# Kernel optimization log

Hardware: AMD Instinct MI355X
Metric: run time of the kernel (lower is better)

Reference implementation:

```python
import jax, jax.numpy as jnp
import numpy as np

NF = 64            # n_filter
CFAC = 3           # SinSobel c_factor: identity + sobel-x + sobel-y
FIN = NF * CFAC    # dyna block input channels (192)
FH = NF * 2        # dyna hidden (128)
FOUT = NF          # dyna output (64)
LAT = 512
N_CALLS = 6        # ceil(log2(128) - log2(2))
P_SIZES = [FH * FIN, FH, FH * FH, FH, FOUT * FH, FOUT, FOUT * FIN, FOUT]
P_TOTAL = sum(P_SIZES)  # 61824
_OFFS = np.cumsum([0] + P_SIZES)

def act(t):
    return jax.nn.leaky_relu(t, 0.2)

def conv1x1(x, w, b):
    # x [B,I,H,W], w [O,I] -> [B,O,H,W]
    return jnp.einsum('bihw,oi->bohw', x, w) + b[None, :, None, None]

def res_block(x, w0, b0, w1, b1):
    # GAN-stability style residual block with 1x1 convs
    return x + 0.1 * conv1x1(act(conv1x1(act(x), w0, b0)), w1, b1)

def depthwise3x3(x, k2d):
    C = x.shape[1]
    k = jnp.broadcast_to(k2d.astype(x.dtype), (C, 1, 3, 3))
    return jax.lax.conv_general_dilated(
        x, k, (1, 1), [(1, 1), (1, 1)],
        dimension_numbers=('NCHW', 'OIHW', 'NCHW'),
        feature_group_count=C)

SOBEL_X = jnp.array([[1., 0., -1.], [2., 0., -2.], [1., 0., -1.]], jnp.float32) / 8.0
SOBEL_Y = SOBEL_X.T
_g = jnp.exp(-0.5 * jnp.array([-1., 0., 1.], jnp.float32) ** 2)
GAUSS = jnp.outer(_g, _g)
GAUSS = GAUSS / GAUSS.sum()

def sin_sobel(x):
    return jnp.concatenate([x, depthwise3x3(x, SOBEL_X), depthwise3x3(x, SOBEL_Y)], axis=1)

def dyna_residual(x, params):
    # per-sample hypernetwork-generated 1x1-conv residual block
    B = x.shape[0]
    def take(i, shape):
        return params[:, _OFFS[i]:_OFFS[i + 1]].reshape((B,) + shape)
    w_in, b_in = take(0, (FH, FIN)), take(1, (FH,))
    w_mid, b_mid = take(2, (FH, FH)), take(3, (FH,))
    w_out, b_out = take(4, (FOUT, FH)), take(5, (FOUT,))
    w_sk, b_sk = take(6, (FOUT, FIN)), take(7, (FOUT,))
    def pconv(h, w, b):  # batched per-sample 1x1 conv
        return jnp.einsum('bihw,boi->bohw', h, w) + b[:, :, None, None]
    x_s = pconv(x, w_sk, b_sk)
    dx = pconv(x, w_in, b_in)
    dx = pconv(act(dx), w_mid, b_mid)
    dx = pconv(act(dx), w_out, b_out)
    return x_s + dx

def downsample(x):
    # GaussianSmoothing(k=3, sigma=1, pad=1) then bilinear 0.5
    # (align_corners=False bilinear at scale 0.5 == 2x2 average pooling)
    x = depthwise3x3(x, GAUSS)
    B, C, H, W = x.shape
    return x.reshape(B, C, H // 2, 2, W // 2, 2).mean(axis=(3, 5))

def lin_res(x, w1, b1, w2, b2, sw=None, sb=None):
    x_s = x if sw is None else x @ sw + sb
    return x_s + 0.1 * (act(act(x) @ w1 + b1) @ w2 + b2)

def forward(x, inj_lat, leak, in_w, in_b, inrb_w0, inrb_b0, inrb_w1, inrb_b1,
            hyp_w, hyp_b, outrb_w0, outrb_b0, outrb_w1, outrb_b1,
            l1_sw, l1_sb, l1_w1, l1_b1, l1_w2, l1_b2,
            l2_w1, l2_b1, l2_w2, l2_b2, lo_w, lo_b):
    out = conv1x1(x, in_w, in_b)
    out = res_block(out, inrb_w0, inrb_b0, inrb_w1, inrb_b1)
    leak_f = jnp.clip(leak, 0.001, 1000.0)
    dyn_params = inj_lat @ hyp_w + hyp_b  # [B, P_TOTAL], shared across calls
    out_embs = [out]
    for _ in range(N_CALLS):  # fixed small layer loop; spatial dims halve each call
        out_new = sin_sobel(out)
        out_new = dyna_residual(out_new, dyn_params)
        out = out + leak_f * out_new
        out = downsample(out)
        out_embs.append(out)
    out = res_block(out, outrb_w0, outrb_b0, outrb_w1, outrb_b1)
    h = out.mean(axis=(2, 3))  # [B, NF]
    h = lin_res(h, l1_w1, l1_b1, l1_w2, l1_b2, l1_sw, l1_sb)
    h = lin_res(h, l2_w1, l2_b1, l2_w2, l2_b2)
    lat = h @ lo_w + lo_b
    return lat, out_embs

def setup_inputs() -> dict:
    key = jax.random.key(0)
    ks = jax.random.split(key, 24)
    B, C, S = 8, 3, 128
    def rn(k, shape, scale=0.05):
        return scale * jax.random.normal(k, shape, jnp.float32)
    z = lambda n: jnp.zeros((n,), jnp.float32)
    return {
        'x': jax.random.normal(ks[0], (B, C, S, S), jnp.float32),
        'inj_lat': jax.random.normal(ks[1], (B, LAT), jnp.float32),
        'leak': jnp.array(0.1, jnp.float32),
        'in_w': rn(ks[2], (NF, C)), 'in_b': z(NF),
        'inrb_w0': rn(ks[3], (NF, NF)), 'inrb_b0': z(NF),
        'inrb_w1': rn(ks[4], (NF, NF)), 'inrb_b1': z(NF),
        'hyp_w': rn(ks[5], (LAT, P_TOTAL), 0.01), 'hyp_b': rn(ks[6], (P_TOTAL,), 0.01),
        'outrb_w0': rn(ks[7], (NF, NF)), 'outrb_b0': z(NF),
        'outrb_w1': rn(ks[8], (NF, NF)), 'outrb_b1': z(NF),
        'l1_sw': rn(ks[9], (NF, LAT)), 'l1_sb': z(LAT),
        'l1_w1': rn(ks[10], (NF, 2 * LAT)), 'l1_b1': z(2 * LAT),
        'l1_w2': rn(ks[11], (2 * LAT, LAT)), 'l1_b2': z(LAT),
        'l2_w1': rn(ks[12], (LAT, LAT)), 'l2_b1': z(LAT),
        'l2_w2': rn(ks[13], (LAT, LAT)), 'l2_b2': z(LAT),
        'lo_w': rn(ks[14], (LAT, LAT)), 'lo_b': z(LAT),
    }

def reference(x, inj_lat, leak, in_w, in_b, inrb_w0, inrb_b0, inrb_w1, inrb_b1,
              hyp_w, hyp_b, outrb_w0, outrb_b0, outrb_w1, outrb_b1,
              l1_sw, l1_sb, l1_w1, l1_b1, l1_w2, l1_b2,
              l2_w1, l2_b1, l2_w2, l2_b2, lo_w, lo_b):
    lat, out_embs = forward(x, inj_lat, leak, in_w, in_b, inrb_w0, inrb_b0, inrb_w1, inrb_b1,
                            hyp_w, hyp_b, outrb_w0, outrb_b0, outrb_w1, outrb_b1,
                            l1_sw, l1_sb, l1_w1, l1_b1, l1_w2, l1_b2,
                            l2_w1, l2_b1, l2_w2, l2_b2, lo_w, lo_b)
    return (lat, *out_embs)
```

## Files before the change

### kernel.cpp

```cpp
#include <hip/hip_runtime.h>


#define BATCH 8
#define PT 61824

typedef __attribute__((ext_vector_type(8))) short bf16x8;
typedef __attribute__((ext_vector_type(4))) float f32x4;

__device__ __forceinline__ float lrelu(float v) { return v > 0.f ? v : 0.2f * v; }

__device__ __forceinline__ short f2bf(float f) {
    union { float fv; unsigned u; } v; v.fv = f;
    return (short)((v.u + 0x7fffu + ((v.u >> 16) & 1u)) >> 16);
}

__global__ __launch_bounds__(256) void hyper_kernel(
    const float* __restrict__ inj, const float* __restrict__ hw,
    const float* __restrict__ hb, float* __restrict__ dyn,
    short* __restrict__ dyn16)
{
    __shared__ float s_l[512 * 8];
    int t = threadIdx.x;
    for (int i = t; i < 4096; i += 256) {
        int b = i >> 9, k = i & 511;
        s_l[k * 8 + b] = inj[i];
    }
    __syncthreads();
    int p = blockIdx.x * 256 + t;
    if (p >= PT) return;
    float acc[8];
#pragma unroll
    for (int b = 0; b < 8; ++b) acc[b] = 0.f;
    for (int k = 0; k < 512; ++k) {
        float w = hw[(size_t)k * PT + p];
        float4 a0 = *(const float4*)&s_l[k * 8];
        float4 a1 = *(const float4*)&s_l[k * 8 + 4];
        acc[0] += a0.x * w; acc[1] += a0.y * w; acc[2] += a0.z * w; acc[3] += a0.w * w;
        acc[4] += a1.x * w; acc[5] += a1.y * w; acc[6] += a1.z * w; acc[7] += a1.w * w;
    }
    float bias = hb[p];
#pragma unroll
    for (int b = 0; b < 8; ++b) {
        float v = acc[b] + bias;
        dyn[(size_t)b * PT + p] = v;
        dyn16[(size_t)b * PT + p] = f2bf(v);
    }
}

__global__ __launch_bounds__(256) void stem_kernel(
    const float* __restrict__ x, const float* __restrict__ in_w,
    const float* __restrict__ in_b,
    const float* __restrict__ w0, const float* __restrict__ b0,
    const float* __restrict__ w1, const float* __restrict__ b1,
    float* __restrict__ out0)
{
    const int HW = 128 * 128;
    __shared__ float s_t0[64 * 68];
    __shared__ short s_vh[2 * 64 * 72];
    __shared__ float s_x[192];
    short* s_v = s_vh;
    short* s_h = s_vh + 64 * 72;
    float* s_y = (float*)s_vh;

    const int b = blockIdx.x >> 8;
    const int tile = blockIdx.x & 255;
    const int pix0 = tile * 64;
    const int t = threadIdx.x;
    const int l = t & 63, w = t >> 6;
    const int lp = l & 15, lq = l >> 4;

    if (t < 192) s_x[t] = x[(size_t)b * 3 * HW + (t >> 6) * HW + pix0 + (t & 63)];
    __syncthreads();

    for (int j = t; j < 1024; j += 256) {
        int p = j & 63, cg = j >> 6;
        float x0 = s_x[p], x1 = s_x[64 + p], x2 = s_x[128 + p];
        short pk[4];
#pragma unroll
        for (int cc = 0; cc < 4; ++cc) {
            int c = cg * 4 + cc;
            float v = in_b[c] + x0 * in_w[c * 3] + x1 * in_w[c * 3 + 1]
                    + x2 * in_w[c * 3 + 2];
            s_t0[c * 68 + p] = v;
            pk[cc] = f2bf(lrelu(v));
        }
        *(short4*)&s_v[p * 72 + cg * 4] = make_short4(pk[0], pk[1], pk[2], pk[3]);
    }
    __syncthreads();

    const int o = w * 16 + lp;
    const f32x4 z4 = {0.f, 0.f, 0.f, 0.f};

    bf16x8 wb0[2], wb1[2];
#pragma unroll
    for (int k = 0; k < 2; ++k) {
        bf16x8 p0, p1;
#pragma unroll
        for (int e = 0; e < 8; ++e) {
            p0[e] = f2bf(w0[o * 64 + k * 32 + lq * 8 + e]);
            p1[e] = f2bf(w1[o * 64 + k * 32 + lq * 8 + e]);
        }
        wb0[k] = p0; wb1[k] = p1;
    }

    {
        f32x4 acc[4];
#pragma unroll
        for (int mt = 0; mt < 4; ++mt) acc[mt] = z4;
#pragma unroll
        for (int k = 0; k < 2; ++k)
#pragma unroll
            for (int mt = 0; mt < 4; ++mt) {
                bf16x8 a = *(const bf16x8*)&s_v[(mt * 16 + lp) * 72 + k * 32 + lq * 8];
                acc[mt] = __builtin_amdgcn_mfma_f32_16x16x32_bf16(a, wb0[k], acc[mt], 0, 0, 0);
            }
        float bi = b0[o];
#pragma unroll
        for (int mt = 0; mt < 4; ++mt)
#pragma unroll
            for (int r = 0; r < 4; ++r)
                s_h[(mt * 16 + lq * 4 + r) * 72 + o] = f2bf(lrelu(acc[mt][r] + bi));
    }
    __syncthreads();

    {
        f32x4 acc[4];
#pragma unroll
        for (int mt = 0; mt < 4; ++mt) acc[mt] = z4;
#pragma unroll
        for (int k = 0; k < 2; ++k)
#pragma unroll
            for (int mt = 0; mt < 4; ++mt) {
                bf16x8 a = *(const bf16x8*)&s_h[(mt * 16 + lp) * 72 + k * 32 + lq * 8];
                acc[mt] = __builtin_amdgcn_mfma_f32_16x16x32_bf16(a, wb1[k], acc[mt], 0, 0, 0);
            }
        float bi = b1[o];
        __syncthreads();
#pragma unroll
        for (int mt = 0; mt < 4; ++mt) {
            f32x4 dv;
#pragma unroll
            for (int r = 0; r < 4; ++r) dv[r] = 0.1f * (acc[mt][r] + bi);
            *(f32x4*)&s_y[o * 68 + mt * 16 + lq * 4] = dv;
        }
    }
    __syncthreads();

#pragma unroll
    for (int v = 0; v < 4; ++v) {
        int idx = v * 1024 + t * 4;
        int oo = idx >> 6, px = idx & 63;
        f32x4 t0v = *(const f32x4*)&s_t0[oo * 68 + px];
        f32x4 dv = *(const f32x4*)&s_y[oo * 68 + px];
        f32x4 ov = t0v + dv;
        *(f32x4*)&out0[((size_t)b * 64 + oo) * HW + pix0 + px] = ov;
    }
}

template<int MT>
__global__ __launch_bounds__(256) void iter_kernel(
    const float* __restrict__ cur, const float* __restrict__ dynf,
    const short* __restrict__ dynb, const float* __restrict__ leak_p,
    float* __restrict__ y, int S, int sh)
{
    constexpr int PX = MT * 16;
    constexpr int SY = (MT == 4) ? 68 : 20;
    __shared__ short s_s[PX * 200];
    __shared__ short s_h[PX * 136];
    float* s_y = (float*)s_s;

    const int HW = S * S;
    const int tilesPer = HW / PX;
    const int b = blockIdx.x / tilesPer;
    const int tile = blockIdx.x - b * tilesPer;
    const int pix0 = tile * PX;
    const int t = threadIdx.x;
    const int l = t & 63, w = t >> 6;
    const int lp = l & 15, lq = l >> 4;
    const float* base = cur + (size_t)b * 64 * HW;

    {
        const int p = (MT == 4) ? (lp + 16 * w) : lp;
        const int gpx = pix0 + p;
        const int row = gpx >> sh;
        const int x = gpx & (S - 1);
        const bool rm = (row > 0), rp = (row < S - 1);
        const bool le = (lp == 0) && (x > 0);
        const bool re = (lp == 15) && (x < S - 1);
        const int iters = (MT == 4) ? 8 : 2;
        int* s32 = (int*)s_s;
        for (int i = 0; i < iters; ++i) {
            const int cp = (MT == 4) ? (lq + 4 * i) : (lq + 4 * w + 16 * i);
            unsigned pk_id = 0, pk_sx = 0, pk_sy = 0;
#pragma unroll
            for (int cc = 0; cc < 2; ++cc) {
                const int c = 2 * cp + cc;
                const float* ch = base + (size_t)c * HW + row * S;
                float vm = rm ? ch[x - S] : 0.f;
                float v0 = ch[x];
                float vp = rp ? ch[x + S] : 0.f;
                float elm = 0.f, el0 = 0.f, elp = 0.f, erm = 0.f, er0 = 0.f, erp = 0.f;
                if (le) { elm = rm ? ch[x - 1 - S] : 0.f; el0 = ch[x - 1]; elp = rp ? ch[x - 1 + S] : 0.f; }
                if (re) { erm = rm ? ch[x + 1 - S] : 0.f; er0 = ch[x + 1]; erp = rp ? ch[x + 1 + S] : 0.f; }
                float Lm = __shfl(vm, l - 1), L0 = __shfl(v0, l - 1), Lp = __shfl(vp, l - 1);
                float Rm = __shfl(vm, l + 1), R0 = __shfl(v0, l + 1), Rp = __shfl(vp, l + 1);
                if (lp == 0)  { Lm = elm; L0 = el0; Lp = elp; }
                if (lp == 15) { Rm = erm; R0 = er0; Rp = erp; }
                if (x == 0)     { Lm = 0.f; L0 = 0.f; Lp = 0.f; }
                if (x == S - 1) { Rm = 0.f; R0 = 0.f; Rp = 0.f; }
                float sx = (Lm - Rm + 2.f * (L0 - R0) + Lp - Rp) * 0.125f;
                float sy = (Lm + 2.f * vm + Rm - Lp - 2.f * vp - Rp) * 0.125f;
                unsigned hid = (unsigned short)f2bf(v0);
                unsigned hsx = (unsigned short)f2bf(sx);
                unsigned hsy = (unsigned short)f2bf(sy);
                pk_id |= hid << (16 * cc);
                pk_sx |= hsx << (16 * cc);
                pk_sy |= hsy << (16 * cc);
            }
            s32[p * 100 + cp] = (int)pk_id;
            s32[p * 100 + 32 + cp] = (int)pk_sx;
            s32[p * 100 + 64 + cp] = (int)pk_sy;
        }
    }
    __syncthreads();

    const short* wb = dynb + (size_t)b * PT;
    const float* pf = dynf + (size_t)b * PT;
    const f32x4 z4 = {0.f, 0.f, 0.f, 0.f};

    f32x4 acc_sk[MT];
#pragma unroll
    for (int mt = 0; mt < MT; ++mt) acc_sk[mt] = z4;

    {
        f32x4 acc[2][MT];
#pragma unroll
        for (int n = 0; n < 2; ++n)
#pragma unroll
            for (int mt = 0; mt < MT; ++mt) acc[n][mt] = z4;
        const int osk = w * 16 + lp;
        for (int k = 0; k < 6; ++k) {
            bf16x8 a[MT];
#pragma unroll
            for (int mt = 0; mt < MT; ++mt)
                a[mt] = *(const bf16x8*)&s_s[(mt * 16 + lp) * 200 + k * 32 + lq * 8];
#pragma unroll
            for (int n = 0; n < 2; ++n) {
                int o = (w * 2 + n) * 16 + lp;
                bf16x8 bb = *(const bf16x8*)&wb[o * 192 + k * 32 + lq * 8];
#pragma unroll
                for (int mt = 0; mt < MT; ++mt)
                    acc[n][mt] = __builtin_amdgcn_mfma_f32_16x16x32_bf16(a[mt], bb, acc[n][mt], 0, 0, 0);
            }
            {
                bf16x8 bsk = *(const bf16x8*)&wb[49472 + osk * 192 + k * 32 + lq * 8];
#pragma unroll
                for (int mt = 0; mt < MT; ++mt)
                    acc_sk[mt] = __builtin_amdgcn_mfma_f32_16x16x32_bf16(a[mt], bsk, acc_sk[mt], 0, 0, 0);
            }
        }
#pragma unroll
        for (int n = 0; n < 2; ++n) {
            int o = (w * 2 + n) * 16 + lp;
            float bi = pf[24576 + o];
#pragma unroll
            for (int mt = 0; mt < MT; ++mt)
#pragma unroll
                for (int r = 0; r < 4; ++r)
                    s_h[(mt * 16 + lq * 4 + r) * 136 + o] = f2bf(lrelu(acc[n][mt][r] + bi));
        }
    }
    __syncthreads();

    {
        f32x4 acc[2][MT];
#pragma unroll
        for (int n = 0; n < 2; ++n)
#pragma unroll
            for (int mt = 0; mt < MT; ++mt) acc[n][mt] = z4;
        for (int k = 0; k < 4; ++k) {
            bf16x8 a[MT];
#pragma unroll
            for (int mt = 0; mt < MT; ++mt)
                a[mt] = *(const bf16x8*)&s_h[(mt * 16 + lp) * 136 + k * 32 + lq * 8];
#pragma unroll
            for (int n = 0; n < 2; ++n) {
                int o = (w * 2 + n) * 16 + lp;
                bf16x8 bb = *(const bf16x8*)&wb[24704 + o * 128 + k * 32 + lq * 8];
#pragma unroll
                for (int mt = 0; mt < MT; ++mt)
                    acc[n][mt] = __builtin_amdgcn_mfma_f32_16x16x32_bf16(a[mt], bb, acc[n][mt], 0, 0, 0);
            }
        }
        __syncthreads();
#pragma unroll
        for (int n = 0; n < 2; ++n) {
            int o = (w * 2 + n) * 16 + lp;
            float bi = pf[41088 + o];
#pragma unroll
            for (int mt = 0; mt < MT; ++mt)
#pragma unroll
                for (int r = 0; r < 4; ++r)
                    s_h[(mt * 16 + lq * 4 + r) * 136 + o] = f2bf(lrelu(acc[n][mt][r] + bi));
        }
    }
    __syncthreads();

    {
        f32x4 acc[MT];
#pragma unroll
        for (int mt = 0; mt < MT; ++mt) acc[mt] = acc_sk[mt];
        int o = w * 16 + lp;
        for (int k = 0; k < 4; ++k) {
            bf16x8 bb = *(const bf16x8*)&wb[41216 + o * 128 + k * 32 + lq * 8];
#pragma unroll
            for (int mt = 0; mt < MT; ++mt) {
                bf16x8 a = *(const bf16x8*)&s_h[(mt * 16 + lp) * 136 + k * 32 + lq * 8];
                acc[mt] = __builtin_amdgcn_mfma_f32_16x16x32_bf16(a, bb, acc[mt], 0, 0, 0);
            }
        }
        float bi = pf[49408 + o] + pf[61760 + o];
#pragma unroll
        for (int mt = 0; mt < MT; ++mt)
#pragma unroll
            for (int r = 0; r < 4; ++r)
                s_y[o * SY + mt * 16 + lq * 4 + r] = acc[mt][r] + bi;
    }
    __syncthreads();

    {
        float lk = fminf(fmaxf(leak_p[0], 0.001f), 1000.f);
        if (MT == 4) {
#pragma unroll
            for (int v = 0; v < 4; ++v) {
                int idx = v * 1024 + t * 4;
                int o = idx >> 6, px = idx & 63;
                f32x4 sv = *(const f32x4*)&s_y[o * SY + px];
                const float* cb = cur + ((size_t)b * 64 + o) * HW + pix0 + px;
                float* yb = y + ((size_t)b * 64 + o) * HW + pix0 + px;
                f32x4 cv = *(const f32x4*)cb;
                *(f32x4*)yb = cv + lk * sv;
            }
        } else {
            int o = t >> 2, px = (t & 3) * 4;
            f32x4 sv = *(const f32x4*)&s_y[o * SY + px];
            const float* cb = cur + ((size_t)b * 64 + o) * HW + pix0 + px;
            float* yb = y + ((size_t)b * 64 + o) * HW + pix0 + px;
            f32x4 cv = *(const f32x4*)cb;
            *(f32x4*)yb = cv + lk * sv;
        }
    }
}

__global__ __launch_bounds__(256) void down_kernel(
    const float* __restrict__ yin, float* __restrict__ outp,
    int S, int S2, int TW, int CPB, int tiles)
{
    __shared__ float s_in[3072];
    __shared__ float s_hb[1152];

    const float ga = 0.60653065971263342f;
    const float gs = 1.f / ((1.f + 2.f * ga) * (1.f + 2.f * ga));
    const float u0 = ga, u1 = 1.f + ga;

    const int t = threadIdx.x;
    const int bi = blockIdx.x;
    const int tix = bi % tiles;
    const int rem = bi / tiles;
    const int tiy = rem % tiles;
    const int cg = rem / tiles;
    const int bc0 = cg * CPB;

    const int IH = 2 * TW + 2;
    const int IW = IH;
    const int IWP = IW + 2;
    const int HS = TW + 1;
    const int gy0 = tiy * 2 * TW - 1;
    const int gx0 = tix * 2 * TW - 1;

    const int loadTot = CPB * IH * IW;
    for (int j = t; j < loadTot; j += 256) {
        int c = j / (IH * IW);
        int r = j - c * (IH * IW);
        int iy = r / IW, ix = r - iy * IW;
        int gy = gy0 + iy, gx = gx0 + ix;
        float v = 0.f;
        if (gy >= 0 && gy < S && gx >= 0 && gx < S)
            v = yin[(size_t)(bc0 + c) * S * S + gy * S + gx];
        s_in[(c * IH + iy) * IWP + ix] = v;
    }
    __syncthreads();

    const int hTot = CPB * IH * TW;
    for (int j = t; j < hTot; j += 256) {
        int c = j / (IH * TW);
        int r = j - c * (IH * TW);
        int iy = r / TW, ox = r - iy * TW;
        const float* pin = &s_in[(c * IH + iy) * IWP + 2 * ox];
        s_hb[(c * IH + iy) * HS + ox] =
            u0 * (pin[0] + pin[3]) + u1 * (pin[1] + pin[2]);
    }
    __syncthreads();

    {
        int ox = t % TW;
        int r = t / TW;
        int oy = r % TW;
        int c = r / TW;
        const float* ph = &s_hb[(c * IH + 2 * oy) * HS + ox];
        float acc = u0 * (ph[0] + ph[3 * HS]) + u1 * (ph[HS] + ph[2 * HS]);
        outp[(size_t)(bc0 + c) * S2 * S2 + (tiy * TW + oy) * S2 + tix * TW + ox] =
            acc * 0.25f * gs;
    }
}

__global__ __launch_bounds__(256) void head_a_kernel(
    const float* __restrict__ emb6,
    const float* __restrict__ w0, const float* __restrict__ b0,
    const float* __restrict__ w1, const float* __restrict__ b1,
    float* __restrict__ h)
{
    __shared__ float sm_t[256], sm_v[256], sm_r[256];
    int b = blockIdx.x, t = threadIdx.x;
    sm_t[t] = emb6[b * 256 + t];
    __syncthreads();
    {
        int o = t & 63, p = t >> 6;
        float acc = 0.f;
        for (int k = 0; k < 64; ++k) acc += w0[o * 64 + k] * lrelu(sm_t[k * 4 + p]);
        sm_v[o * 4 + p] = lrelu(acc + b0[o]);
    }
    __syncthreads();
    {
        int o = t & 63, p = t >> 6;
        float acc = 0.f;
        for (int k = 0; k < 64; ++k) acc += w1[o * 64 + k] * sm_v[k * 4 + p];
        sm_r[o * 4 + p] = sm_t[o * 4 + p] + 0.1f * (acc + b1[o]);
    }
    __syncthreads();
    if (t < 64)
        h[b * 64 + t] = 0.25f * (sm_r[t * 4] + sm_r[t * 4 + 1] + sm_r[t * 4 + 2] + sm_r[t * 4 + 3]);
}

__global__ __launch_bounds__(256) void head_b_kernel(
    const float* __restrict__ h, const float* __restrict__ w,
    const float* __restrict__ bias, float* __restrict__ t1)
{
    __shared__ float s_h[64];
    int id = blockIdx.x * 256 + threadIdx.x;
    int b = id >> 10, o = id & 1023;
    if (threadIdx.x < 64) s_h[threadIdx.x] = lrelu(h[b * 64 + threadIdx.x]);
    __syncthreads();
    float acc = 0.f;
    for (int k = 0; k < 64; ++k) acc += s_h[k] * w[k * 1024 + o];
    t1[b * 1024 + o] = lrelu(acc + bias[o]);
}

__global__ __launch_bounds__(256) void head_c_kernel(
    const float* __restrict__ h, const float* __restrict__ t1,
    const float* __restrict__ sw, const float* __restrict__ sb,
    const float* __restrict__ w2, const float* __restrict__ b2,
    float* __restrict__ h1)
{
    __shared__ float s_t[8 * 128];
    __shared__ float s_h[8 * 64];
    int oblk = blockIdx.x & 1, chunk = blockIdx.x >> 1;
    int t = threadIdx.x;
    int o = oblk * 256 + t;
    for (int j = t; j < 1024; j += 256) {
        int b = j >> 7, kk = j & 127;
        s_t[j] = t1[b * 1024 + chunk * 128 + kk];
    }
    if (chunk == 0)
        for (int j = t; j < 512; j += 256) s_h[j] = h[j];
    __syncthreads();
    float acc[8];
#pragma unroll
    for (int b = 0; b < 8; ++b) acc[b] = 0.f;
    for (int kk = 0; kk < 128; ++kk) {
        float wv = w2[(chunk * 128 + kk) * 512 + o];
#pragma unroll
        for (int b = 0; b < 8; ++b) acc[b] += s_t[b * 128 + kk] * wv;
    }
#pragma unroll
    for (int b = 0; b < 8; ++b) acc[b] *= 0.1f;
    if (chunk == 0) {
        for (int k = 0; k < 64; ++k) {
            float wv = sw[k * 512 + o];
#pragma unroll
            for (int b = 0; b < 8; ++b) acc[b] += s_h[b * 64 + k] * wv;
        }
        float c0 = sb[o] + 0.1f * b2[o];
#pragma unroll
        for (int b = 0; b < 8; ++b) acc[b] += c0;
    }
#pragma unroll
    for (int b = 0; b < 8; ++b) atomicAdd(&h1[b * 512 + o], acc[b]);
}

__global__ __launch_bounds__(256) void head_d_kernel(
    const float* __restrict__ h1, const float* __restrict__ w,
    const float* __restrict__ bias, float* __restrict__ z3)
{
    __shared__ float s_u[8 * 64];
    int oblk = blockIdx.x & 1, chunk = blockIdx.x >> 1;
    int t = threadIdx.x;
    int o = oblk * 256 + t;
    for (int j = t; j < 512; j += 256) {
        int b = j >> 6, kk = j & 63;
        s_u[j] = lrelu(h1[b * 512 + chunk * 64 + kk]);
    }
    __syncthreads();
    float acc[8];
#pragma unroll
    for (int b = 0; b < 8; ++b) acc[b] = 0.f;
    for (int kk = 0; kk < 64; ++kk) {
        float wv = w[(chunk * 64 + kk) * 512 + o];
#pragma unroll
        for (int b = 0; b < 8; ++b) acc[b] += s_u[b * 64 + kk] * wv;
    }
    if (chunk == 0) {
        float c0 = bias[o];
#pragma unroll
        for (int b = 0; b < 8; ++b) acc[b] += c0;
    }
#pragma unroll
    for (int b = 0; b < 8; ++b) atomicAdd(&z3[b * 512 + o], acc[b]);
}

__global__ __launch_bounds__(256) void head_e_kernel(
    const float* __restrict__ h1, const float* __restrict__ z3,
    const float* __restrict__ w, const float* __restrict__ bias,
    float* __restrict__ h2)
{
    __shared__ float s_u[8 * 64];
    int oblk = blockIdx.x & 1, chunk = blockIdx.x >> 1;
    int t = threadIdx.x;
    int o = oblk * 256 + t;
    for (int j = t; j < 512; j += 256) {
        int b = j >> 6, kk = j & 63;
        s_u[j] = lrelu(z3[b * 512 + chunk * 64 + kk]);
    }
    __syncthreads();
    float acc[8];
#pragma unroll
    for (int b = 0; b < 8; ++b) acc[b] = 0.f;
    for (int kk = 0; kk < 64; ++kk) {
        float wv = w[(chunk * 64 + kk) * 512 + o];
#pragma unroll
        for (int b = 0; b < 8; ++b) acc[b] += s_u[b * 64 + kk] * wv;
    }
#pragma unroll
    for (int b = 0; b < 8; ++b) acc[b] *= 0.1f;
    if (chunk == 0) {
        float c0 = 0.1f * bias[o];
#pragma unroll
        for (int b = 0; b < 8; ++b) acc[b] += h1[b * 512 + o] + c0;
    }
#pragma unroll
    for (int b = 0; b < 8; ++b) atomicAdd(&h2[b * 512 + o], acc[b]);
}

__global__ __launch_bounds__(256) void head_f_kernel(
    const float* __restrict__ h2, const float* __restrict__ w,
    const float* __restrict__ bias, float* __restrict__ lat)
{
    __shared__ float s_u[8 * 64];
    int oblk = blockIdx.x & 1, chunk = blockIdx.x >> 1;
    int t = threadIdx.x;
    int o = oblk * 256 + t;
    for (int j = t; j < 512; j += 256) {
        int b = j >> 6, kk = j & 63;
        s_u[j] = h2[b * 512 + chunk * 64 + kk];
    }
    __syncthreads();
    float acc[8];
#pragma unroll
    for (int b = 0; b < 8; ++b) acc[b] = 0.f;
    for (int kk = 0; kk < 64; ++kk) {
        float wv = w[(chunk * 64 + kk) * 512 + o];
#pragma unroll
        for (int b = 0; b < 8; ++b) acc[b] += s_u[b * 64 + kk] * wv;
    }
    if (chunk == 0) {
        float c0 = bias[o];
#pragma unroll
        for (int b = 0; b < 8; ++b) acc[b] += c0;
    }
#pragma unroll
    for (int b = 0; b < 8; ++b) atomicAdd(&lat[b * 512 + o], acc[b]);
}

extern "C" void kernel_launch(void* const* d_in, const int* in_sizes, int n_in,
                              void* d_out, int out_size, void* d_ws, size_t ws_size,
                              hipStream_t stream) {
    const float* x      = (const float*)d_in[0];
    const float* inj    = (const float*)d_in[1];
    const float* leak   = (const float*)d_in[2];
    const float* in_w   = (const float*)d_in[3];
    const float* in_b   = (const float*)d_in[4];
    const float* inrb_w0 = (const float*)d_in[5];
    const float* inrb_b0 = (const float*)d_in[6];
    const float* inrb_w1 = (const float*)d_in[7];
    const float* inrb_b1 = (const float*)d_in[8];
    const float* hyp_w  = (const float*)d_in[9];
    const float* hyp_b  = (const float*)d_in[10];
    const float* outrb_w0 = (const float*)d_in[11];
    const float* outrb_b0 = (const float*)d_in[12];
    const float* outrb_w1 = (const float*)d_in[13];
    const float* outrb_b1 = (const float*)d_in[14];
    const float* l1_sw  = (const float*)d_in[15];
    const float* l1_sb  = (const float*)d_in[16];
    const float* l1_w1  = (const float*)d_in[17];
    const float* l1_b1  = (const float*)d_in[18];
    const float* l1_w2  = (const float*)d_in[19];
    const float* l1_b2  = (const float*)d_in[20];
    const float* l2_w1  = (const float*)d_in[21];
    const float* l2_b1  = (const float*)d_in[22];
    const float* l2_w2  = (const float*)d_in[23];
    const float* l2_b2  = (const float*)d_in[24];
    const float* lo_w   = (const float*)d_in[25];
    const float* lo_b   = (const float*)d_in[26];

    float* out = (float*)d_out;
    float* dyn = (float*)d_ws;
    float* ybuf = dyn + (size_t)BATCH * PT;
    short* dyn16 = (short*)(ybuf + (size_t)BATCH * 64 * 16384);
    float* hbuf = (float*)(dyn16 + (size_t)BATCH * PT);
    float* t1buf = hbuf + 512;
    float* h1buf = t1buf + 8192;
    float* z3buf = h1buf + 4096;
    float* h2buf = z3buf + 4096;

    hipMemsetAsync(h1buf, 0, (4096 * 3) * sizeof(float), stream);
    hipMemsetAsync(out, 0, 4096 * sizeof(float), stream);

    hyper_kernel<<<(PT + 255) / 256, 256, 0, stream>>>(inj, hyp_w, hyp_b, dyn, dyn16);

    size_t cur = 4096;
    stem_kernel<<<BATCH * 256, 256, 0, stream>>>(
        x, in_w, in_b, inrb_w0, inrb_b0, inrb_w1, inrb_b1, out + cur);

    int S = 128, sh = 7;
    for (int i = 0; i < 6; ++i) {
        if (S >= 64) {
            iter_kernel<4><<<BATCH * (S * S / 64), 256, 0, stream>>>(
                out + cur, dyn, dyn16, leak, ybuf, S, sh);
        } else {
            iter_kernel<1><<<BATCH * (S * S / 16), 256, 0, stream>>>(
                out + cur, dyn, dyn16, leak, ybuf, S, sh);
        }
        int S2 = S >> 1;
        size_t nxt = cur + (size_t)BATCH * 64 * S * S;
        int TW = (S2 >= 16) ? 16 : S2;
        int tiles = S2 / TW;
        int CPB = 256 / (TW * TW);
        if (CPB < 1) CPB = 1;
        int grid = (BATCH * 64 / CPB) * tiles * tiles;
        down_kernel<<<grid, 256, 0, stream>>>(ybuf, out + nxt, S, S2, TW, CPB, tiles);
        cur = nxt;
        S = S2; sh -= 1;
    }

    head_a_kernel<<<BATCH, 256, 0, stream>>>(
        out + cur, outrb_w0, outrb_b0, outrb_w1, outrb_b1, hbuf);
    head_b_kernel<<<32, 256, 0, stream>>>(hbuf, l1_w1, l1_b1, t1buf);
    head_c_kernel<<<16, 256, 0, stream>>>(hbuf, t1buf, l1_sw, l1_sb, l1_w2, l1_b2, h1buf);
    head_d_kernel<<<16, 256, 0, stream>>>(h1buf, l2_w1, l2_b1, z3buf);
    head_e_kernel<<<16, 256, 0, stream>>>(h1buf, z3buf, l2_w2, l2_b2, h2buf);
    head_f_kernel<<<16, 256, 0, stream>>>(h2buf, lo_w, lo_b, out);
}
```

Baseline: 529.7 us.

## Split-K hypernet GEMV, XOR-swizzle iter LDS tiles, remap workgroups across XCDs

The hypernet kernel now splits the 512-long K reduction across four wavefronts, with 64 outputs per block and a shared-memory reduction, which launches about four times as many blocks and raises parallelism for the weight stream. The iteration kernel drops padded LDS rows in favour of an XOR swizzle on the perception and hidden tiles, meant to avoid bank conflicts while using less LDS, and stores the final tile with vector writes. Both the iteration and downsample kernels remap block IDs so consecutive logical tiles are spread across the 8 XCDs. The remap assumes the grid size is divisible by 8, and the swizzle index math adds some ALU work.

```diff
diff --git a/kernel.cpp b/kernel.cpp
--- a/kernel.cpp
+++ b/kernel.cpp
@@ -20,30 +20,39 @@
     short* __restrict__ dyn16)
 {
     __shared__ float s_l[512 * 8];
+    __shared__ float s_part[3 * 8 * 64];
     int t = threadIdx.x;
     for (int i = t; i < 4096; i += 256) {
         int b = i >> 9, k = i & 511;
         s_l[k * 8 + b] = inj[i];
     }
     __syncthreads();
-    int p = blockIdx.x * 256 + t;
-    if (p >= PT) return;
+    int po = t & 63, kq = t >> 6;
+    int p = blockIdx.x * 64 + po;
     float acc[8];
 #pragma unroll
     for (int b = 0; b < 8; ++b) acc[b] = 0.f;
-    for (int k = 0; k < 512; ++k) {
+    for (int k = kq * 128; k < kq * 128 + 128; ++k) {
         float w = hw[(size_t)k * PT + p];
         float4 a0 = *(const float4*)&s_l[k * 8];
         float4 a1 = *(const float4*)&s_l[k * 8 + 4];
         acc[0] += a0.x * w; acc[1] += a0.y * w; acc[2] += a0.z * w; acc[3] += a0.w * w;
         acc[4] += a1.x * w; acc[5] += a1.y * w; acc[6] += a1.z * w; acc[7] += a1.w * w;
     }
-    float bias = hb[p];
-#pragma unroll
-    for (int b = 0; b < 8; ++b) {
-        float v = acc[b] + bias;
-        dyn[(size_t)b * PT + p] = v;
-        dyn16[(size_t)b * PT + p] = f2bf(v);
+    if (kq > 0) {
+#pragma unroll
+        for (int b = 0; b < 8; ++b) s_part[((kq - 1) * 8 + b) * 64 + po] = acc[b];
+    }
+    __syncthreads();
+    if (kq == 0) {
+        float bias = hb[p];
+#pragma unroll
+        for (int b = 0; b < 8; ++b) {
+            float v = acc[b] + s_part[b * 64 + po] + s_part[(8 + b) * 64 + po]
+                    + s_part[(16 + b) * 64 + po] + bias;
+            dyn[(size_t)b * PT + p] = v;
+            dyn16[(size_t)b * PT + p] = f2bf(v);
+        }
     }
 }
 
@@ -165,14 +174,17 @@
 {
     constexpr int PX = MT * 16;
     constexpr int SY = (MT == 4) ? 68 : 20;
-    __shared__ short s_s[PX * 200];
-    __shared__ short s_h[PX * 136];
+    __shared__ short s_s[PX * 192];
+    __shared__ short s_h[PX * 128];
     float* s_y = (float*)s_s;
 
     const int HW = S * S;
     const int tilesPer = HW / PX;
-    const int b = blockIdx.x / tilesPer;
-    const int tile = blockIdx.x - b * tilesPer;
+    const int nwg = BATCH * tilesPer;
+    const int rb = (int)blockIdx.x;
+    const int lb = (rb & 7) * (nwg >> 3) + (rb >> 3);
+    const int b = lb / tilesPer;
+    const int tile = lb - b * tilesPer;
     const int pix0 = tile * PX;
     const int t = threadIdx.x;
     const int l = t & 63, w = t >> 6;
@@ -181,6 +193,7 @@
 
     {
         const int p = (MT == 4) ? (lp + 16 * w) : lp;
+        const int rxw = (p & 7) << 2;
         const int gpx = pix0 + p;
         const int row = gpx >> sh;
         const int x = gpx & (S - 1);
@@ -217,9 +230,10 @@
                 pk_sx |= hsx << (16 * cc);
                 pk_sy |= hsy << (16 * cc);
             }
-            s32[p * 100 + cp] = (int)pk_id;
-            s32[p * 100 + 32 + cp] = (int)pk_sx;
-            s32[p * 100 + 64 + cp] = (int)pk_sy;
+            const int cpx_ = cp ^ rxw;
+            s32[p * 96 + cpx_] = (int)pk_id;
+            s32[p * 96 + 32 + cpx_] = (int)pk_sx;
+            s32[p * 96 + 64 + cpx_] = (int)pk_sy;
         }
     }
     __syncthreads();
@@ -227,6 +241,10 @@
     const short* wb = dynb + (size_t)b * PT;
     const float* pf = dynf + (size_t)b * PT;
     const f32x4 z4 = {0.f, 0.f, 0.f, 0.f};
+    const int sx4 = (lp & 7) << 4;
+    const char* ss_b = (const char*)s_s;
+    const char* sh_cb = (const char*)s_h;
+    char* sh_b = (char*)s_h;
 
     f32x4 acc_sk[MT];
 #pragma unroll
@@ -243,7 +261,7 @@
             bf16x8 a[MT];
 #pragma unroll
             for (int mt = 0; mt < MT; ++mt)
-                a[mt] = *(const bf16x8*)&s_s[(mt * 16 + lp) * 200 + k * 32 + lq * 8];
+                a[mt] = *(const bf16x8*)(ss_b + (mt * 16 + lp) * 384 + ((k * 64 + lq * 16) ^ sx4));
 #pragma unroll
             for (int n = 0; n < 2; ++n) {
                 int o = (w * 2 + n) * 16 + lp;
@@ -266,8 +284,11 @@
 #pragma unroll
             for (int mt = 0; mt < MT; ++mt)
 #pragma unroll
-                for (int r = 0; r < 4; ++r)
-                    s_h[(mt * 16 + lq * 4 + r) * 136 + o] = f2bf(lrelu(acc[n][mt][r] + bi));
+                for (int r = 0; r < 4; ++r) {
+                    int row = mt * 16 + lq * 4 + r;
+                    *(short*)(sh_b + row * 256 + ((o * 2) ^ ((row & 7) << 4))) =
+                        f2bf(lrelu(acc[n][mt][r] + bi));
+                }
         }
     }
     __syncthreads();
@@ -282,7 +303,7 @@
             bf16x8 a[MT];
 #pragma unroll
             for (int mt = 0; mt < MT; ++mt)
-                a[mt] = *(const bf16x8*)&s_h[(mt * 16 + lp) * 136 + k * 32 + lq * 8];
+                a[mt] = *(const bf16x8*)(sh_cb + (mt * 16 + lp) * 256 + ((k * 64 + lq * 16) ^ sx4));
 #pragma unroll
             for (int n = 0; n < 2; ++n) {
                 int o = (w * 2 + n) * 16 + lp;
@@ -300,8 +321,11 @@
 #pragma unroll
             for (int mt = 0; mt < MT; ++mt)
 #pragma unroll
-                for (int r = 0; r < 4; ++r)
-                    s_h[(mt * 16 + lq * 4 + r) * 136 + o] = f2bf(lrelu(acc[n][mt][r] + bi));
+                for (int r = 0; r < 4; ++r) {
+                    int row = mt * 16 + lq * 4 + r;
+                    *(short*)(sh_b + row * 256 + ((o * 2) ^ ((row & 7) << 4))) =
+                        f2bf(lrelu(acc[n][mt][r] + bi));
+                }
         }
     }
     __syncthreads();
@@ -315,16 +339,18 @@
             bf16x8 bb = *(const bf16x8*)&wb[41216 + o * 128 + k * 32 + lq * 8];
 #pragma unroll
             for (int mt = 0; mt < MT; ++mt) {
-                bf16x8 a = *(const bf16x8*)&s_h[(mt * 16 + lp) * 136 + k * 32 + lq * 8];
+                bf16x8 a = *(const bf16x8*)(sh_cb + (mt * 16 + lp) * 256 + ((k * 64 + lq * 16) ^ sx4));
                 acc[mt] = __builtin_amdgcn_mfma_f32_16x16x32_bf16(a, bb, acc[mt], 0, 0, 0);
             }
         }
         float bi = pf[49408 + o] + pf[61760 + o];
 #pragma unroll
-        for (int mt = 0; mt < MT; ++mt)
-#pragma unroll
-            for (int r = 0; r < 4; ++r)
-                s_y[o * SY + mt * 16 + lq * 4 + r] = acc[mt][r] + bi;
+        for (int mt = 0; mt < MT; ++mt) {
+            f32x4 dv;
+#pragma unroll
+            for (int r = 0; r < 4; ++r) dv[r] = acc[mt][r] + bi;
+            *(f32x4*)&s_y[o * SY + mt * 16 + lq * 4] = dv;
+        }
     }
     __syncthreads();
 
@@ -364,7 +390,9 @@
     const float u0 = ga, u1 = 1.f + ga;
 
     const int t = threadIdx.x;
-    const int bi = blockIdx.x;
+    const int nwg = (int)gridDim.x;
+    const int rb = (int)blockIdx.x;
+    const int bi = (rb & 7) * (nwg >> 3) + (rb >> 3);
     const int tix = bi % tiles;
     const int rem = bi / tiles;
     const int tiy = rem % tiles;
@@ -635,7 +663,7 @@
     hipMemsetAsync(h1buf, 0, (4096 * 3) * sizeof(float), stream);
     hipMemsetAsync(out, 0, 4096 * sizeof(float), stream);
 
-    hyper_kernel<<<(PT + 255) / 256, 256, 0, stream>>>(inj, hyp_w, hyp_b, dyn, dyn16);
+    hyper_kernel<<<PT / 64, 256, 0, stream>>>(inj, hyp_w, hyp_b, dyn, dyn16);
 
     size_t cur = 4096;
     stem_kernel<<<BATCH * 256, 256, 0, stream>>>(
```

Result: faster. 516.0 us (-2.6%).
